# Performance work log

Measured on AMD Instinct MI355X. Metric: run time of the kernel, lower is better.

Reference implementation:

```python
import jax, jax.numpy as jnp
import numpy as np

B, T, E, D = 8, 2048, 1024, 128


def setup_inputs() -> dict:
    key = jax.random.key(0)
    k1, k2, k3, k4 = jax.random.split(key, 4)
    x = jax.random.normal(k1, (B, T, E), dtype=jnp.float32)
    wq = jax.random.normal(k2, (E, D), dtype=jnp.float32) * (E ** -0.5)
    wk = jax.random.normal(k3, (E, D), dtype=jnp.float32) * (E ** -0.5)
    wv = jax.random.normal(k4, (E, D), dtype=jnp.float32) * (E ** -0.5)
    return {"x": x, "wq": wq, "wk": wk, "wv": wv}


def reference(x, wq, wk, wv):
    # Projections (bias-free Linear): [B,T,E] @ [E,D] -> [B,T,D]
    q = x @ wq
    k = x @ wk
    v = x @ wv
    d = k.shape[-1]
    # Faithful to source: scores / d**(-0.5) == scores * sqrt(d)
    scores = jnp.einsum('btd,bsd->bts', q, k) * (d ** 0.5)
    causal = jnp.tril(jnp.ones((x.shape[1], x.shape[1]), dtype=bool))
    scores = jnp.where(causal, scores, -jnp.inf)
    weights = jax.nn.softmax(scores, axis=-1)  # dropout omitted (eval mode)
    return jnp.einsum('bts,bsd->btd', weights, v)
```

## Files before the change

### kernel.cpp

```cpp
#include <hip/hip_runtime.h>


#define NB 8
#define NT 2048
#define NE 1024
#define ND 128

typedef unsigned short U16;
typedef unsigned int U32;
typedef __attribute__((ext_vector_type(8))) short vbf8;
typedef __attribute__((ext_vector_type(4))) float vf4;

#define EXP2F(x) __builtin_amdgcn_exp2f(x)

__device__ __forceinline__ U16 f2bf(float f) {
  U32 u = __builtin_bit_cast(U32, f);
  u += 0x7fffu + ((u >> 16) & 1u);
  return (U16)(u >> 16);
}
__device__ __forceinline__ float bf2f(U16 h) {
  U32 u = ((U32)h) << 16;
  return __builtin_bit_cast(float, u);
}
__device__ __forceinline__ void gl_lds16(const void* g, void* l) {
  __builtin_amdgcn_global_load_lds((__attribute__((address_space(1))) void*)g,
                                   (__attribute__((address_space(3))) void*)l, 16, 0, 0);
}

__global__ void wsplit_kernel(const float* __restrict__ wq, const float* __restrict__ wk,
                              const float* __restrict__ wv, U16* __restrict__ wth,
                              U16* __restrict__ wtl) {
  int id = blockIdx.x * 256 + threadIdx.x;
  if (id >= 384 * 1024) return;
  int n = id >> 10, e = id & 1023;
  float v;
  if (n < 128)      v = wq[e * 128 + n] * 16.322231701033217f;
  else if (n < 256) v = wk[e * 128 + (n - 128)];
  else              v = wv[e * 128 + (n - 256)];
  U16 h = f2bf(v);
  wth[id] = h;
  wtl[id] = f2bf(v - bf2f(h));
}

__global__ __launch_bounds__(256, 3) void qkv_kernel(
    const float* __restrict__ x, const U16* __restrict__ wth, const U16* __restrict__ wtl,
    U16* __restrict__ qfh, U16* __restrict__ qfl, U16* __restrict__ kfh,
    U16* __restrict__ kfl, U16* __restrict__ vf) {
  __shared__ __align__(16) char smem[49152];
  char* Ah = smem;
  char* Al = smem + 8192;
  char* Bh = smem + 16384;
  char* Bl = smem + 32768;

  const int tid = threadIdx.x;
  const int w = tid >> 6, lane = tid & 63;
  const int fr = lane & 15, fq = lane >> 4;
  const int m0 = blockIdx.x * 64;
  const int nt = blockIdx.y;
  const U16* bh_src = wth + nt * (128 * 1024);
  const U16* bl_src = wtl + nt * (128 * 1024);

  const vf4 vzero = {0.f, 0.f, 0.f, 0.f};
  vf4 acc[2][4];
#pragma unroll
  for (int i = 0; i < 2; ++i)
#pragma unroll
    for (int j = 0; j < 4; ++j) acc[i][j] = vzero;

  const int wm = (w >> 1) * 32, wn = (w & 1) * 64;
  const int arow = tid >> 2, ag = tid & 3;

  for (int k0 = 0; k0 < 1024; k0 += 64) {
#pragma unroll
    for (int p = 0; p < 4; ++p) {
      const int g = p * 256 + tid;
      const int row = g >> 3, c = g & 7;
      const int sc = c ^ (row & 7);
      const int ldsb = (p * 256 + w * 64) * 16;
      gl_lds16(bh_src + row * 1024 + k0 + sc * 8, Bh + ldsb);
      if (nt < 2) gl_lds16(bl_src + row * 1024 + k0 + sc * 8, Bl + ldsb);
    }
    {
      const float* s = x + (size_t)(m0 + arow) * 1024 + k0 + ag * 8;
      float v0[8], v1[8];
      ((float4*)v0)[0] = *(const float4*)(s);
      ((float4*)v0)[1] = *(const float4*)(s + 4);
      ((float4*)v1)[0] = *(const float4*)(s + 32);
      ((float4*)v1)[1] = *(const float4*)(s + 36);
      vbf8 h0, l0, h1, l1;
#pragma unroll
      for (int i = 0; i < 8; ++i) {
        U16 a = f2bf(v0[i]);
        h0[i] = (short)a; l0[i] = (short)f2bf(v0[i] - bf2f(a));
        U16 b = f2bf(v1[i]);
        h1[i] = (short)b; l1[i] = (short)f2bf(v1[i] - bf2f(b));
      }
      const int sw = arow & 7;
      *(vbf8*)(Ah + arow * 128 + ((ag ^ sw) << 4))       = h0;
      *(vbf8*)(Ah + arow * 128 + (((ag + 4) ^ sw) << 4)) = h1;
      if (nt < 2) {
        *(vbf8*)(Al + arow * 128 + ((ag ^ sw) << 4))       = l0;
        *(vbf8*)(Al + arow * 128 + (((ag + 4) ^ sw) << 4)) = l1;
      }
    }
    __syncthreads();

    if (nt < 2) {
#pragma unroll
      for (int kc = 0; kc < 2; ++kc) {
        vbf8 a_h[2], a_l[2], b_h[4], b_l[4];
#pragma unroll
        for (int i = 0; i < 2; ++i) {
          const int row = wm + i * 16 + fr;
          const int off = row * 128 + (((kc * 4 + fq) ^ (row & 7)) << 4);
          a_h[i] = *(const vbf8*)(Ah + off);
          a_l[i] = *(const vbf8*)(Al + off);
        }
#pragma unroll
        for (int j = 0; j < 4; ++j) {
          const int row = wn + j * 16 + fr;
          const int off = row * 128 + (((kc * 4 + fq) ^ (row & 7)) << 4);
          b_h[j] = *(const vbf8*)(Bh + off);
          b_l[j] = *(const vbf8*)(Bl + off);
        }
#pragma unroll
        for (int i = 0; i < 2; ++i)
#pragma unroll
          for (int j = 0; j < 4; ++j) {
            acc[i][j] = __builtin_amdgcn_mfma_f32_16x16x32_bf16(a_h[i], b_h[j], acc[i][j], 0, 0, 0);
            acc[i][j] = __builtin_amdgcn_mfma_f32_16x16x32_bf16(a_h[i], b_l[j], acc[i][j], 0, 0, 0);
            acc[i][j] = __builtin_amdgcn_mfma_f32_16x16x32_bf16(a_l[i], b_h[j], acc[i][j], 0, 0, 0);
          }
      }
    } else {
#pragma unroll
      for (int kc = 0; kc < 2; ++kc) {
        vbf8 a_h[2], b_h[4];
#pragma unroll
        for (int i = 0; i < 2; ++i) {
          const int row = wm + i * 16 + fr;
          a_h[i] = *(const vbf8*)(Ah + row * 128 + (((kc * 4 + fq) ^ (row & 7)) << 4));
        }
#pragma unroll
        for (int j = 0; j < 4; ++j) {
          const int row = wn + j * 16 + fr;
          b_h[j] = *(const vbf8*)(Bh + row * 128 + (((kc * 4 + fq) ^ (row & 7)) << 4));
        }
#pragma unroll
        for (int i = 0; i < 2; ++i)
#pragma unroll
          for (int j = 0; j < 4; ++j)
            acc[i][j] = __builtin_amdgcn_mfma_f32_16x16x32_bf16(a_h[i], b_h[j], acc[i][j], 0, 0, 0);
      }
    }
    __syncthreads();
  }

  const int b = m0 >> 11;
  if (nt < 2) {
    U16* tlh = (U16*)smem;
    U16* tll = (U16*)(smem + 16896);
#pragma unroll
    for (int i = 0; i < 2; ++i)
#pragma unroll
      for (int j = 0; j < 4; ++j)
#pragma unroll
        for (int r = 0; r < 4; ++r) {
          const int ml = wm + i * 16 + fq * 4 + r;
          const int col = wn + j * 16 + fr;
          const float val = acc[i][j][r];
          const U16 h = f2bf(val);
          tlh[ml * 132 + col] = h;
          tll[ml * 132 + col] = f2bf(val - bf2f(h));
        }
    __syncthreads();
    U16* dh = (nt == 0) ? qfh : kfh;
    U16* dl = (nt == 0) ? qfl : kfl;
    const int g0 = (m0 & 2047) >> 4;
#pragma unroll
    for (int p = 0; p < 4; ++p) {
      const int idx = p * 256 + tid;
      const int gl = idx >> 8, kc = (idx >> 6) & 3, ln = idx & 63;
      const int row = gl * 16 + (ln & 15);
      const int colc = kc * 32 + (ln >> 4) * 8;
      const size_t o = (((size_t)b * 128 + g0 + gl) * 4 + kc) * 512 + ln * 8;
      *(vbf8*)(dh + o) = *(const vbf8*)(tlh + row * 132 + colc);
      *(vbf8*)(dl + o) = *(const vbf8*)(tll + row * 132 + colc);
    }
  } else {
    U16* tl = (U16*)smem;
#pragma unroll
    for (int i = 0; i < 2; ++i)
#pragma unroll
      for (int j = 0; j < 4; ++j)
#pragma unroll
        for (int r = 0; r < 4; ++r) {
          const int ml = wm + i * 16 + fq * 4 + r;
          const int col = wn + j * 16 + fr;
          tl[col * 68 + ml] = f2bf(acc[i][j][r]);
        }
    __syncthreads();
    const int sc0 = (m0 & 2047) >> 5;
#pragma unroll
    for (int p = 0; p < 4; ++p) {
      const int idx = p * 256 + tid;
      const int df = idx >> 7, sc = (idx >> 6) & 1, ln = idx & 63;
      const int d = df * 16 + (ln & 15);
      const int sl = sc * 32 + (ln >> 4) * 8;
      const size_t o = (((size_t)b * 8 + df) * 64 + (sc0 + sc)) * 512 + ln * 8;
      *(vbf8*)(vf + o) = *(const vbf8*)(tl + d * 68 + sl);
    }
  }
}

__global__ __launch_bounds__(256, 3) void flash_kernel(
    const U16* __restrict__ qfh, const U16* __restrict__ qfl,
    const U16* __restrict__ kfh, const U16* __restrict__ kfl,
    const U16* __restrict__ vf, float* __restrict__ out) {
  __shared__ __align__(16) char smem[25088];

  const int tid = threadIdx.x;
  const int w = tid >> 6, lane = tid & 63;
  const int fr = lane & 15, fq = lane >> 4;
  const int sq = w;
  const int bid = blockIdx.x;
  const int bb = bid & 7;
  const int jj = bid >> 3;
  const int g = (jj < 64) ? (127 - jj) : (jj - 64);
  const int q0g = g * 16;

  vbf8 q_h[4], q_l[4];
  {
    const U16* qb = qfh + ((size_t)bb * 128 + g) * 2048 + lane * 8;
    const U16* qlb = qfl + ((size_t)bb * 128 + g) * 2048 + lane * 8;
#pragma unroll
    for (int kc = 0; kc < 4; ++kc) {
      q_h[kc] = *(const vbf8*)(qb + kc * 512);
      q_l[kc] = *(const vbf8*)(qlb + kc * 512);
    }
  }

  const U16* khp = kfh + (size_t)bb * 262144 + (size_t)(sq * 4) * 2048 + lane * 8;
  const U16* klp = kfl + (size_t)bb * 262144 + (size_t)(sq * 4) * 2048 + lane * 8;
  const U16* vfp = vf + (size_t)bb * 262144 + (size_t)(sq * 2) * 512 + lane * 8;
  U16* pw = (U16*)(smem + w * 2304);

  const vf4 vzero = {0.f, 0.f, 0.f, 0.f};
  vf4 oacc[8];
#pragma unroll
  for (int i = 0; i < 8; ++i) oacc[i] = vzero;
  float m_r[4], l_r[4];
#pragma unroll
  for (int r = 0; r < 4; ++r) { m_r[r] = -__builtin_inff(); l_r[r] = 0.f; }

  const int lim = q0g + 15 - sq * 64;
  const int ntw = (lim >= 0) ? ((lim >> 8) + 1) : 0;

  for (int T = 0; T < ntw; ++T) {
    vf4 sacc[4] = {vzero, vzero, vzero, vzero};
    __builtin_amdgcn_s_setprio(1);
#pragma unroll
    for (int sf = 0; sf < 4; ++sf) {
#pragma unroll
      for (int kc = 0; kc < 4; ++kc) {
        const vbf8 kh_r = *(const vbf8*)(khp + sf * 2048 + kc * 512);
        const vbf8 kl_r = *(const vbf8*)(klp + sf * 2048 + kc * 512);
        sacc[sf] = __builtin_amdgcn_mfma_f32_16x16x32_bf16(q_h[kc], kh_r, sacc[sf], 0, 0, 0);
        sacc[sf] = __builtin_amdgcn_mfma_f32_16x16x32_bf16(q_h[kc], kl_r, sacc[sf], 0, 0, 0);
        sacc[sf] = __builtin_amdgcn_mfma_f32_16x16x32_bf16(q_l[kc], kh_r, sacc[sf], 0, 0, 0);
      }
    }
    __builtin_amdgcn_s_setprio(0);

    if (T == ntw - 1) {
#pragma unroll
      for (int sf = 0; sf < 4; ++sf) {
        const int s_g = T * 256 + sq * 64 + sf * 16 + fr;
#pragma unroll
        for (int r = 0; r < 4; ++r)
          if (s_g > q0g + fq * 4 + r) sacc[sf][r] = -__builtin_inff();
      }
    }

    float tmax[4];
#pragma unroll
    for (int r = 0; r < 4; ++r)
      tmax[r] = fmaxf(fmaxf(sacc[0][r], sacc[1][r]), fmaxf(sacc[2][r], sacc[3][r]));
#pragma unroll
    for (int off = 1; off < 16; off <<= 1)
#pragma unroll
      for (int r = 0; r < 4; ++r) tmax[r] = fmaxf(tmax[r], __shfl_xor(tmax[r], off, 64));

    vbf8 vreg[8][2];
#pragma unroll
    for (int df = 0; df < 8; ++df) {
      vreg[df][0] = *(const vbf8*)(vfp + df * 32768);
      vreg[df][1] = *(const vbf8*)(vfp + df * 32768 + 512);
    }

    bool need = false;
    float mne[4];
#pragma unroll
    for (int r = 0; r < 4; ++r) {
      need |= (tmax[r] > m_r[r]);
      const float mn = fmaxf(m_r[r], tmax[r]);
      mne[r] = (mn == -__builtin_inff()) ? 0.f : mn;
    }
    if (__any(need)) {
#pragma unroll
      for (int r = 0; r < 4; ++r) {
        const float alpha = EXP2F(m_r[r] - mne[r]);
        l_r[r] *= alpha;
        m_r[r] = fmaxf(m_r[r], tmax[r]);
#pragma unroll
        for (int i = 0; i < 8; ++i) oacc[i][r] *= alpha;
      }
    }

    float psum[4];
    U16 pb[4][4];
#pragma unroll
    for (int sf = 0; sf < 4; ++sf)
#pragma unroll
      for (int r = 0; r < 4; ++r) {
        const float pv = EXP2F(sacc[sf][r] - mne[r]);
        psum[r] = (sf == 0) ? pv : (psum[r] + pv);
        pb[sf][r] = f2bf(pv);
      }
#pragma unroll
    for (int off = 1; off < 16; off <<= 1)
#pragma unroll
      for (int r = 0; r < 4; ++r) psum[r] += __shfl_xor(psum[r], off, 64);
#pragma unroll
    for (int r = 0; r < 4; ++r) l_r[r] += psum[r];

#pragma unroll
    for (int sf = 0; sf < 4; ++sf)
#pragma unroll
      for (int r = 0; r < 4; ++r) pw[(fq * 4 + r) * 72 + sf * 16 + fr] = pb[sf][r];
    asm volatile("s_waitcnt lgkmcnt(0)" ::: "memory");
    const vbf8 pf0 = *(const vbf8*)(pw + fr * 72 + fq * 8);
    const vbf8 pf1 = *(const vbf8*)(pw + fr * 72 + 32 + fq * 8);

    __builtin_amdgcn_s_setprio(1);
#pragma unroll
    for (int df = 0; df < 8; ++df) {
      oacc[df] = __builtin_amdgcn_mfma_f32_16x16x32_bf16(pf0, vreg[df][0], oacc[df], 0, 0, 0);
      oacc[df] = __builtin_amdgcn_mfma_f32_16x16x32_bf16(pf1, vreg[df][1], oacc[df], 0, 0, 0);
    }
    __builtin_amdgcn_s_setprio(0);

    khp += 32768; klp += 32768; vfp += 4096;
  }

  __syncthreads();
  float* O_d = (float*)smem;
  float* m_s = (float*)(smem + 24576);
  float* l_s = (float*)(smem + 24832);
  if (sq > 0) {
#pragma unroll
    for (int i = 0; i < 8; ++i)
#pragma unroll
      for (int r = 0; r < 4; ++r)
        O_d[((sq - 1) * 16 + fq * 4 + r) * 128 + i * 16 + fr] = oacc[i][r];
  }
  if (fr == 0) {
#pragma unroll
    for (int r = 0; r < 4; ++r) {
      m_s[sq * 16 + fq * 4 + r] = m_r[r];
      l_s[sq * 16 + fq * 4 + r] = l_r[r];
    }
  }
  __syncthreads();
  if (sq == 0) {
#pragma unroll
    for (int r = 0; r < 4; ++r) {
      const int row = fq * 4 + r;
      float mv[4];
      float M = -__builtin_inff();
#pragma unroll
      for (int p = 0; p < 4; ++p) {
        mv[p] = m_s[p * 16 + row];
        M = fmaxf(M, mv[p]);
      }
      float wgt[4], denom = 0.f;
#pragma unroll
      for (int p = 0; p < 4; ++p) {
        wgt[p] = EXP2F(mv[p] - M);
        denom += wgt[p] * l_s[p * 16 + row];
      }
      const float inv = 1.f / denom;
#pragma unroll
      for (int i = 0; i < 8; ++i) {
        float o = wgt[0] * oacc[i][r];
#pragma unroll
        for (int p = 1; p < 4; ++p)
          o += wgt[p] * O_d[((p - 1) * 16 + row) * 128 + i * 16 + fr];
        out[(size_t)(bb * 2048 + q0g + row) * 128 + i * 16 + fr] = o * inv;
      }
    }
  }
}

extern "C" void kernel_launch(void* const* d_in, const int* in_sizes, int n_in, void* d_out,
                              int out_size, void* d_ws, size_t ws_size, hipStream_t stream) {
  const float* x = (const float*)d_in[0];
  const float* wq = (const float*)d_in[1];
  const float* wk = (const float*)d_in[2];
  const float* wv = (const float*)d_in[3];
  char* ws = (char*)d_ws;
  U16* wth = (U16*)(ws);
  U16* wtl = (U16*)(ws + 786432);
  U16* qfh = (U16*)(ws + 1572864);
  U16* qfl = (U16*)(ws + 5767168);
  U16* kfh = (U16*)(ws + 9961472);
  U16* kfl = (U16*)(ws + 14155776);
  U16* vfr = (U16*)(ws + 18350080);
  float* out = (float*)d_out;

  wsplit_kernel<<<dim3(1536), dim3(256), 0, stream>>>(wq, wk, wv, wth, wtl);
  qkv_kernel<<<dim3(256, 3), dim3(256), 0, stream>>>(x, wth, wtl, qfh, qfl, kfh, kfl, vfr);
  flash_kernel<<<dim3(1024), dim3(256), 0, stream>>>(qfh, qfl, kfh, kfl, vfr, out);
}
```

Before: 94.07 us.

## Process 32 query rows per flash block to reuse K/V fragments

Each flash block now handles two 16-row query fragments (32 rows) instead of one, and each wave covers 32 keys per 128-key step instead of 64 per 256-key step. Every K and V register fragment loaded from global memory then feeds MFMAs for both query fragments, halving K/V load traffic per query row. The cost is twice the accumulator and Q registers, doubled LDS for the cross-wave merge, launch bounds dropped to 2 blocks per CU, and half as many blocks, which lowers occupancy and latency hiding.

```diff
diff --git a/kernel.cpp b/kernel.cpp
--- a/kernel.cpp
+++ b/kernel.cpp
@@ -213,11 +213,11 @@
   }
 }
 
-__global__ __launch_bounds__(256, 3) void flash_kernel(
+__global__ __launch_bounds__(256, 2) void flash_kernel(
     const U16* __restrict__ qfh, const U16* __restrict__ qfl,
     const U16* __restrict__ kfh, const U16* __restrict__ kfl,
     const U16* __restrict__ vf, float* __restrict__ out) {
-  __shared__ __align__(16) char smem[25088];
+  __shared__ __align__(16) char smem[50176];
 
   const int tid = threadIdx.x;
   const int w = tid >> 6, lane = tid & 63;
@@ -226,179 +226,209 @@
   const int bid = blockIdx.x;
   const int bb = bid & 7;
   const int jj = bid >> 3;
-  const int g = (jj < 64) ? (127 - jj) : (jj - 64);
-  const int q0g = g * 16;
-
-  vbf8 q_h[4], q_l[4];
-  {
-    const U16* qb = qfh + ((size_t)bb * 128 + g) * 2048 + lane * 8;
-    const U16* qlb = qfl + ((size_t)bb * 128 + g) * 2048 + lane * 8;
+  const int qt = (bid < 256) ? (63 - jj) : (jj - 32);
+  const int q0g = qt * 32;
+
+  vbf8 q_h[2][4], q_l[2][4];
+#pragma unroll
+  for (int qf = 0; qf < 2; ++qf) {
+    const U16* qb  = qfh + ((size_t)bb * 128 + qt * 2 + qf) * 2048 + lane * 8;
+    const U16* qlb = qfl + ((size_t)bb * 128 + qt * 2 + qf) * 2048 + lane * 8;
 #pragma unroll
     for (int kc = 0; kc < 4; ++kc) {
-      q_h[kc] = *(const vbf8*)(qb + kc * 512);
-      q_l[kc] = *(const vbf8*)(qlb + kc * 512);
-    }
-  }
-
-  const U16* khp = kfh + (size_t)bb * 262144 + (size_t)(sq * 4) * 2048 + lane * 8;
-  const U16* klp = kfl + (size_t)bb * 262144 + (size_t)(sq * 4) * 2048 + lane * 8;
-  const U16* vfp = vf + (size_t)bb * 262144 + (size_t)(sq * 2) * 512 + lane * 8;
-  U16* pw = (U16*)(smem + w * 2304);
+      q_h[qf][kc] = *(const vbf8*)(qb + kc * 512);
+      q_l[qf][kc] = *(const vbf8*)(qlb + kc * 512);
+    }
+  }
+
+  const U16* khp = kfh + (size_t)bb * 262144 + (size_t)(sq * 2) * 2048 + lane * 8;
+  const U16* klp = kfl + (size_t)bb * 262144 + (size_t)(sq * 2) * 2048 + lane * 8;
+  const U16* vfp = vf + (size_t)bb * 262144 + (size_t)sq * 512 + lane * 8;
+  U16* pw = (U16*)(smem + w * 2560);
 
   const vf4 vzero = {0.f, 0.f, 0.f, 0.f};
-  vf4 oacc[8];
-#pragma unroll
-  for (int i = 0; i < 8; ++i) oacc[i] = vzero;
-  float m_r[4], l_r[4];
-#pragma unroll
-  for (int r = 0; r < 4; ++r) { m_r[r] = -__builtin_inff(); l_r[r] = 0.f; }
-
-  const int lim = q0g + 15 - sq * 64;
-  const int ntw = (lim >= 0) ? ((lim >> 8) + 1) : 0;
+  vf4 oacc[2][8];
+#pragma unroll
+  for (int qf = 0; qf < 2; ++qf)
+#pragma unroll
+    for (int i = 0; i < 8; ++i) oacc[qf][i] = vzero;
+  float m_r[2][4], l_r[2][4];
+#pragma unroll
+  for (int qf = 0; qf < 2; ++qf)
+#pragma unroll
+    for (int r = 0; r < 4; ++r) { m_r[qf][r] = -__builtin_inff(); l_r[qf][r] = 0.f; }
+
+  const int lim = q0g + 31 - sq * 32;
+  const int ntw = (lim >= 0) ? ((lim >> 7) + 1) : 0;
 
   for (int T = 0; T < ntw; ++T) {
-    vf4 sacc[4] = {vzero, vzero, vzero, vzero};
+    vf4 sacc[2][2] = {{vzero, vzero}, {vzero, vzero}};
     __builtin_amdgcn_s_setprio(1);
 #pragma unroll
-    for (int sf = 0; sf < 4; ++sf) {
+    for (int sf = 0; sf < 2; ++sf) {
 #pragma unroll
       for (int kc = 0; kc < 4; ++kc) {
         const vbf8 kh_r = *(const vbf8*)(khp + sf * 2048 + kc * 512);
         const vbf8 kl_r = *(const vbf8*)(klp + sf * 2048 + kc * 512);
-        sacc[sf] = __builtin_amdgcn_mfma_f32_16x16x32_bf16(q_h[kc], kh_r, sacc[sf], 0, 0, 0);
-        sacc[sf] = __builtin_amdgcn_mfma_f32_16x16x32_bf16(q_h[kc], kl_r, sacc[sf], 0, 0, 0);
-        sacc[sf] = __builtin_amdgcn_mfma_f32_16x16x32_bf16(q_l[kc], kh_r, sacc[sf], 0, 0, 0);
+#pragma unroll
+        for (int qf = 0; qf < 2; ++qf) {
+          sacc[qf][sf] = __builtin_amdgcn_mfma_f32_16x16x32_bf16(q_h[qf][kc], kh_r, sacc[qf][sf], 0, 0, 0);
+          sacc[qf][sf] = __builtin_amdgcn_mfma_f32_16x16x32_bf16(q_h[qf][kc], kl_r, sacc[qf][sf], 0, 0, 0);
+          sacc[qf][sf] = __builtin_amdgcn_mfma_f32_16x16x32_bf16(q_l[qf][kc], kh_r, sacc[qf][sf], 0, 0, 0);
+        }
       }
     }
     __builtin_amdgcn_s_setprio(0);
 
     if (T == ntw - 1) {
 #pragma unroll
-      for (int sf = 0; sf < 4; ++sf) {
-        const int s_g = T * 256 + sq * 64 + sf * 16 + fr;
+      for (int qf = 0; qf < 2; ++qf)
+#pragma unroll
+        for (int sf = 0; sf < 2; ++sf) {
+          const int s_g = T * 128 + sq * 32 + sf * 16 + fr;
+#pragma unroll
+          for (int r = 0; r < 4; ++r)
+            if (s_g > q0g + qf * 16 + fq * 4 + r) sacc[qf][sf][r] = -__builtin_inff();
+        }
+    }
+
+    float tmax[2][4];
+#pragma unroll
+    for (int qf = 0; qf < 2; ++qf)
+#pragma unroll
+      for (int r = 0; r < 4; ++r) tmax[qf][r] = fmaxf(sacc[qf][0][r], sacc[qf][1][r]);
+#pragma unroll
+    for (int off = 1; off < 16; off <<= 1)
+#pragma unroll
+      for (int qf = 0; qf < 2; ++qf)
 #pragma unroll
         for (int r = 0; r < 4; ++r)
-          if (s_g > q0g + fq * 4 + r) sacc[sf][r] = -__builtin_inff();
-      }
-    }
-
-    float tmax[4];
-#pragma unroll
-    for (int r = 0; r < 4; ++r)
-      tmax[r] = fmaxf(fmaxf(sacc[0][r], sacc[1][r]), fmaxf(sacc[2][r], sacc[3][r]));
+          tmax[qf][r] = fmaxf(tmax[qf][r], __shfl_xor(tmax[qf][r], off, 64));
+
+    vbf8 vreg[8];
+#pragma unroll
+    for (int df = 0; df < 8; ++df) vreg[df] = *(const vbf8*)(vfp + df * 32768);
+
+    bool need = false;
+    float mne[2][4];
+#pragma unroll
+    for (int qf = 0; qf < 2; ++qf)
+#pragma unroll
+      for (int r = 0; r < 4; ++r) {
+        need |= (tmax[qf][r] > m_r[qf][r]);
+        const float mn = fmaxf(m_r[qf][r], tmax[qf][r]);
+        mne[qf][r] = (mn == -__builtin_inff()) ? 0.f : mn;
+      }
+    if (__any(need)) {
+#pragma unroll
+      for (int qf = 0; qf < 2; ++qf)
+#pragma unroll
+        for (int r = 0; r < 4; ++r) {
+          const float alpha = EXP2F(m_r[qf][r] - mne[qf][r]);
+          l_r[qf][r] *= alpha;
+          m_r[qf][r] = fmaxf(m_r[qf][r], tmax[qf][r]);
+#pragma unroll
+          for (int i = 0; i < 8; ++i) oacc[qf][i][r] *= alpha;
+        }
+    }
+
+    float psum[2][4];
+    U16 pb[2][2][4];
+#pragma unroll
+    for (int qf = 0; qf < 2; ++qf)
+#pragma unroll
+      for (int sf = 0; sf < 2; ++sf)
+#pragma unroll
+        for (int r = 0; r < 4; ++r) {
+          const float pv = EXP2F(sacc[qf][sf][r] - mne[qf][r]);
+          psum[qf][r] = (sf == 0) ? pv : (psum[qf][r] + pv);
+          pb[qf][sf][r] = f2bf(pv);
+        }
 #pragma unroll
     for (int off = 1; off < 16; off <<= 1)
 #pragma unroll
-      for (int r = 0; r < 4; ++r) tmax[r] = fmaxf(tmax[r], __shfl_xor(tmax[r], off, 64));
-
-    vbf8 vreg[8][2];
+      for (int qf = 0; qf < 2; ++qf)
+#pragma unroll
+        for (int r = 0; r < 4; ++r) psum[qf][r] += __shfl_xor(psum[qf][r], off, 64);
+#pragma unroll
+    for (int qf = 0; qf < 2; ++qf)
+#pragma unroll
+      for (int r = 0; r < 4; ++r) l_r[qf][r] += psum[qf][r];
+
+#pragma unroll
+    for (int qf = 0; qf < 2; ++qf)
+#pragma unroll
+      for (int sf = 0; sf < 2; ++sf)
+#pragma unroll
+        for (int r = 0; r < 4; ++r)
+          pw[(qf * 16 + fq * 4 + r) * 40 + sf * 16 + fr] = pb[qf][sf][r];
+    asm volatile("s_waitcnt lgkmcnt(0)" ::: "memory");
+    const vbf8 pf0 = *(const vbf8*)(pw + fr * 40 + fq * 8);
+    const vbf8 pf1 = *(const vbf8*)(pw + (16 + fr) * 40 + fq * 8);
+
+    __builtin_amdgcn_s_setprio(1);
 #pragma unroll
     for (int df = 0; df < 8; ++df) {
-      vreg[df][0] = *(const vbf8*)(vfp + df * 32768);
-      vreg[df][1] = *(const vbf8*)(vfp + df * 32768 + 512);
-    }
-
-    bool need = false;
-    float mne[4];
-#pragma unroll
-    for (int r = 0; r < 4; ++r) {
-      need |= (tmax[r] > m_r[r]);
-      const float mn = fmaxf(m_r[r], tmax[r]);
-      mne[r] = (mn == -__builtin_inff()) ? 0.f : mn;
-    }
-    if (__any(need)) {
-#pragma unroll
-      for (int r = 0; r < 4; ++r) {
-        const float alpha = EXP2F(m_r[r] - mne[r]);
-        l_r[r] *= alpha;
-        m_r[r] = fmaxf(m_r[r], tmax[r]);
-#pragma unroll
-        for (int i = 0; i < 8; ++i) oacc[i][r] *= alpha;
-      }
-    }
-
-    float psum[4];
-    U16 pb[4][4];
-#pragma unroll
-    for (int sf = 0; sf < 4; ++sf)
-#pragma unroll
-      for (int r = 0; r < 4; ++r) {
-        const float pv = EXP2F(sacc[sf][r] - mne[r]);
-        psum[r] = (sf == 0) ? pv : (psum[r] + pv);
-        pb[sf][r] = f2bf(pv);
-      }
-#pragma unroll
-    for (int off = 1; off < 16; off <<= 1)
-#pragma unroll
-      for (int r = 0; r < 4; ++r) psum[r] += __shfl_xor(psum[r], off, 64);
-#pragma unroll
-    for (int r = 0; r < 4; ++r) l_r[r] += psum[r];
-
-#pragma unroll
-    for (int sf = 0; sf < 4; ++sf)
-#pragma unroll
-      for (int r = 0; r < 4; ++r) pw[(fq * 4 + r) * 72 + sf * 16 + fr] = pb[sf][r];
-    asm volatile("s_waitcnt lgkmcnt(0)" ::: "memory");
-    const vbf8 pf0 = *(const vbf8*)(pw + fr * 72 + fq * 8);
-    const vbf8 pf1 = *(const vbf8*)(pw + fr * 72 + 32 + fq * 8);
-
-    __builtin_amdgcn_s_setprio(1);
-#pragma unroll
-    for (int df = 0; df < 8; ++df) {
-      oacc[df] = __builtin_amdgcn_mfma_f32_16x16x32_bf16(pf0, vreg[df][0], oacc[df], 0, 0, 0);
-      oacc[df] = __builtin_amdgcn_mfma_f32_16x16x32_bf16(pf1, vreg[df][1], oacc[df], 0, 0, 0);
+      oacc[0][df] = __builtin_amdgcn_mfma_f32_16x16x32_bf16(pf0, vreg[df], oacc[0][df], 0, 0, 0);
+      oacc[1][df] = __builtin_amdgcn_mfma_f32_16x16x32_bf16(pf1, vreg[df], oacc[1][df], 0, 0, 0);
     }
     __builtin_amdgcn_s_setprio(0);
 
-    khp += 32768; klp += 32768; vfp += 4096;
+    khp += 16384; klp += 16384; vfp += 2048;
   }
 
   __syncthreads();
   float* O_d = (float*)smem;
-  float* m_s = (float*)(smem + 24576);
-  float* l_s = (float*)(smem + 24832);
+  float* m_s = (float*)(smem + 49152);
+  float* l_s = (float*)(smem + 49664);
   if (sq > 0) {
 #pragma unroll
-    for (int i = 0; i < 8; ++i)
-#pragma unroll
-      for (int r = 0; r < 4; ++r)
-        O_d[((sq - 1) * 16 + fq * 4 + r) * 128 + i * 16 + fr] = oacc[i][r];
+    for (int qf = 0; qf < 2; ++qf)
+#pragma unroll
+      for (int i = 0; i < 8; ++i)
+#pragma unroll
+        for (int r = 0; r < 4; ++r)
+          O_d[((sq - 1) * 32 + qf * 16 + fq * 4 + r) * 128 + i * 16 + fr] = oacc[qf][i][r];
   }
   if (fr == 0) {
 #pragma unroll
-    for (int r = 0; r < 4; ++r) {
-      m_s[sq * 16 + fq * 4 + r] = m_r[r];
-      l_s[sq * 16 + fq * 4 + r] = l_r[r];
-    }
+    for (int qf = 0; qf < 2; ++qf)
+#pragma unroll
+      for (int r = 0; r < 4; ++r) {
+        m_s[sq * 32 + qf * 16 + fq * 4 + r] = m_r[qf][r];
+        l_s[sq * 32 + qf * 16 + fq * 4 + r] = l_r[qf][r];
+      }
   }
   __syncthreads();
   if (sq == 0) {
 #pragma unroll
-    for (int r = 0; r < 4; ++r) {
-      const int row = fq * 4 + r;
-      float mv[4];
-      float M = -__builtin_inff();
-#pragma unroll
-      for (int p = 0; p < 4; ++p) {
-        mv[p] = m_s[p * 16 + row];
-        M = fmaxf(M, mv[p]);
-      }
-      float wgt[4], denom = 0.f;
-#pragma unroll
-      for (int p = 0; p < 4; ++p) {
-        wgt[p] = EXP2F(mv[p] - M);
-        denom += wgt[p] * l_s[p * 16 + row];
-      }
-      const float inv = 1.f / denom;
-#pragma unroll
-      for (int i = 0; i < 8; ++i) {
-        float o = wgt[0] * oacc[i][r];
-#pragma unroll
-        for (int p = 1; p < 4; ++p)
-          o += wgt[p] * O_d[((p - 1) * 16 + row) * 128 + i * 16 + fr];
-        out[(size_t)(bb * 2048 + q0g + row) * 128 + i * 16 + fr] = o * inv;
-      }
-    }
+    for (int qf = 0; qf < 2; ++qf)
+#pragma unroll
+      for (int r = 0; r < 4; ++r) {
+        const int row = qf * 16 + fq * 4 + r;
+        float mv[4];
+        float M = -__builtin_inff();
+#pragma unroll
+        for (int p = 0; p < 4; ++p) {
+          mv[p] = m_s[p * 32 + row];
+          M = fmaxf(M, mv[p]);
+        }
+        float wgt[4], denom = 0.f;
+#pragma unroll
+        for (int p = 0; p < 4; ++p) {
+          wgt[p] = EXP2F(mv[p] - M);
+          denom += wgt[p] * l_s[p * 32 + row];
+        }
+        const float inv = 1.f / denom;
+#pragma unroll
+        for (int i = 0; i < 8; ++i) {
+          float o = wgt[0] * oacc[qf][i][r];
+#pragma unroll
+          for (int p = 1; p < 4; ++p)
+            o += wgt[p] * O_d[((p - 1) * 32 + row) * 128 + i * 16 + fr];
+          out[(size_t)(bb * 2048 + q0g + row) * 128 + i * 16 + fr] = o * inv;
+        }
+      }
   }
 }
 
@@ -420,5 +450,5 @@
 
   wsplit_kernel<<<dim3(1536), dim3(256), 0, stream>>>(wq, wk, wv, wth, wtl);
   qkv_kernel<<<dim3(256, 3), dim3(256), 0, stream>>>(x, wth, wtl, qfh, qfl, kfh, kfl, vfr);
-  flash_kernel<<<dim3(1024), dim3(256), 0, stream>>>(qfh, qfl, kfh, kfl, vfr, out);
-}
+  flash_kernel<<<dim3(512), dim3(256), 0, stream>>>(qfh, qfl, kfh, kfl, vfr, out);
+}
```

After: 130.1 us. 38.3% more time.
